# Optimization experiments

Hardware: AMD Instinct MI355X
Metric: run time of the kernel (lower is better)

## Reference

```python
import jax, jax.numpy as jnp
import numpy as np

B, K, D, H = 4, 2048, 768, 12
HD = D // H
NEG = -1e30  # stands in for -inf in the additive mask


def setup_inputs() -> dict:
    key = jax.random.key(0)
    ks = jax.random.split(key, 11)
    s = 1.0 / np.sqrt(D)
    inp = {
        "x": jax.random.normal(ks[0], (B, K, D), jnp.float32),
        "is_context": jax.random.randint(ks[1], (B, K), 0, 2) > 0,
        "Wq": jax.random.normal(ks[2], (D, D), jnp.float32) * s,
        "bq": jax.random.normal(ks[3], (D,), jnp.float32) * 0.01,
        "Wk": jax.random.normal(ks[4], (D, D), jnp.float32) * s,
        "bk": jax.random.normal(ks[5], (D,), jnp.float32) * 0.01,
        "Wv": jax.random.normal(ks[6], (D, D), jnp.float32) * s,
        "bv": jax.random.normal(ks[7], (D,), jnp.float32) * 0.01,
        "Wo": jax.random.normal(ks[8], (D, D), jnp.float32) * s,
        "bo": jax.random.normal(ks[9], (D,), jnp.float32) * 0.01,
    }
    return inp


def reference(x, is_context, Wq, bq, Wk, bk, Wv, bv, Wo, bo):
    b, k_len, d = x.shape
    scale = 1.0 / jnp.sqrt(jnp.asarray(HD, x.dtype))
    # torch nn.Linear: y = x @ W.T + b
    q = (x @ Wq.T + bq).reshape(b, k_len, H, HD).transpose(0, 2, 1, 3)  # [B,H,K,hd]
    kk = (x @ Wk.T + bk).reshape(b, k_len, H, HD).transpose(0, 2, 1, 3)
    v = (x @ Wv.T + bv).reshape(b, k_len, H, HD).transpose(0, 2, 1, 3)

    ctx = is_context  # [B,K] bool
    # allowed[b,i,j]: context rows attend only to context cols; target rows attend to all
    allowed = (ctx[:, :, None] & ctx[:, None, :]) | (~ctx)[:, :, None]  # [B,K,K]

    scores = jnp.einsum("bhqd,bhkd->bhqk", q, kk) * scale  # [B,H,K,K]
    scores = jnp.where(allowed[:, None, :, :], scores, NEG)
    attn = jax.nn.softmax(scores, axis=-1)
    out = jnp.einsum("bhqk,bhkd->bhqd", attn, v)  # [B,H,K,hd]
    out = out.transpose(0, 2, 1, 3).reshape(b, k_len, d)
    return out @ Wo.T + bo
```

## Files before the change

kernel.cpp:

```cpp
#include <hip/hip_runtime.h>
#include <hip/hip_bf16.h>

constexpr int BATCH = 4;
constexpr int SEQ   = 2048;
constexpr int DIM   = 768;
constexpr int NH    = 12;
constexpr int HDIM  = 64;

typedef __attribute__((ext_vector_type(8))) short bf16x8;
typedef __attribute__((ext_vector_type(4))) float f32x4;
typedef __attribute__((ext_vector_type(4))) short s16x4;

__device__ inline short f2bf(float f) {
    union { float f; unsigned u; } v; v.f = f;
    unsigned r = (v.u + 0x7fff + ((v.u >> 16) & 1)) >> 16;
    return (short)r;
}

__device__ inline unsigned pack_bf16x2(float a, float b) {
    union { __hip_bfloat162 h; unsigned u; } c;
    c.h = __float22bfloat162_rn(make_float2(a, b));
    return c.u;
}

__device__ inline float fast_exp2(float x) {
#if __has_builtin(__builtin_amdgcn_exp2f)
    return __builtin_amdgcn_exp2f(x);
#else
    return __expf(x * 0.6931471805599453f);
#endif
}

__device__ inline void gld16(const short* g, short* l) {
    __builtin_amdgcn_global_load_lds(
        (const __attribute__((address_space(1))) void*)g,
        (__attribute__((address_space(3))) void*)l, 16, 0, 0);
}

__device__ inline bool ctx_at(const void* p, bool isU8, int idx) {
    return isU8 ? (((const unsigned char*)p)[idx] != 0)
                : (((const int*)p)[idx] != 0);
}

__global__ __launch_bounds__(256) void prep_kernel(
    const float* __restrict__ x,  const float* __restrict__ Wq,
    const float* __restrict__ Wk, const float* __restrict__ Wv,
    const float* __restrict__ Wo,
    short* __restrict__ xb,  short* __restrict__ Wqb,
    short* __restrict__ Wkb, short* __restrict__ Wvb,
    short* __restrict__ Wob,
    const unsigned char* __restrict__ ctxm, int ctxbytes, int* __restrict__ flag) {
    const int blk = blockIdx.x;
    constexpr int XBLK = (BATCH * SEQ * DIM / 4) / 256;
    constexpr int WBLK = (DIM * DIM / 4) / 256;

    if (blk == XBLK + 4 * WBLK) {
        __shared__ int cnt;
        if (threadIdx.x == 0) cnt = 0;
        __syncthreads();
        int local = 0;
        for (int i = threadIdx.x; i < ctxbytes; i += 256)
            if ((i & 3) != 0 && ctxm[i] != 0) local++;
        atomicAdd(&cnt, local);
        __syncthreads();
        if (threadIdx.x == 0) *flag = (cnt > 0) ? 1 : 0;
        return;
    }

    const float* src; short* dst; int i;
    if (blk < XBLK) {
        src = x; dst = xb;
        i = blk * 256 + threadIdx.x;
    } else {
        const int r = blk - XBLK;
        const int w = r / WBLK;
        src = (w == 0) ? Wq : (w == 1) ? Wk : (w == 2) ? Wv : Wo;
        dst = (w == 0) ? Wqb : (w == 1) ? Wkb : (w == 2) ? Wvb : Wob;
        i = (r - w * WBLK) * 256 + threadIdx.x;
    }
    float4 v = ((const float4*)src)[i];
    s16x4 o;
    o.x = f2bf(v.x); o.y = f2bf(v.y); o.z = f2bf(v.z); o.w = f2bf(v.w);
    ((s16x4*)dst)[i] = o;
}

template <bool BF16OUT>
__global__ __launch_bounds__(256) void gemm_mfma(
    const short* __restrict__ A,
    const short* __restrict__ W0, const float* __restrict__ bias0, void* __restrict__ C0,
    const short* __restrict__ W1, const float* __restrict__ bias1, void* __restrict__ C1,
    const short* __restrict__ W2, const float* __restrict__ bias2, void* __restrict__ C2,
    float scale0) {
    constexpr int N  = DIM;
    constexpr int Kd = DIM;

    const short* W; const float* bias; void* C; float scale;
    if (blockIdx.z == 0)      { W = W0; bias = bias0; C = C0; scale = scale0; }
    else if (blockIdx.z == 1) { W = W1; bias = bias1; C = C1; scale = 1.f; }
    else                      { W = W2; bias = bias2; C = C2; scale = 1.f; }

    const int tid  = threadIdx.x;
    const int wave = tid >> 6;
    const int lane = tid & 63;
    const int quad = lane >> 4;
    const int l16  = lane & 15;
    const int wm   = wave & 1;
    const int wn   = wave >> 1;
    const int m0   = blockIdx.y * 128;
    const int n0   = blockIdx.x * 128;

    __shared__ short As[128 * 32];
    __shared__ short Bs[128 * 32];

    const int srow = tid >> 2;
    const int skq  = tid & 3;
    const short* Ag = A + (size_t)(m0 + srow) * Kd + skq * 8;
    const short* Wg = W + (size_t)(n0 + srow) * Kd + skq * 8;
    short* AsP = As + srow * 32 + skq * 8;
    short* BsP = Bs + srow * 32 + skq * 8;

    f32x4 acc[4][4] = {};

    for (int kt = 0; kt < Kd; kt += 32) {
        __syncthreads();
        gld16(Ag + kt,                AsP);
        gld16(Ag + kt + 64 * Kd,      AsP + 64 * 32);
        gld16(Wg + kt,                BsP);
        gld16(Wg + kt + 64 * Kd,      BsP + 64 * 32);
        __syncthreads();

        bf16x8 af[4], bfr[4];
#pragma unroll
        for (int mt = 0; mt < 4; ++mt)
            af[mt] = *(const bf16x8*)&As[(wm * 64 + mt * 16 + l16) * 32 + quad * 8];
#pragma unroll
        for (int nt = 0; nt < 4; ++nt)
            bfr[nt] = *(const bf16x8*)&Bs[(wn * 64 + nt * 16 + l16) * 32 + quad * 8];
#pragma unroll
        for (int mt = 0; mt < 4; ++mt)
#pragma unroll
            for (int nt = 0; nt < 4; ++nt)
                acc[mt][nt] = __builtin_amdgcn_mfma_f32_16x16x32_bf16(
                    af[mt], bfr[nt], acc[mt][nt], 0, 0, 0);
    }

    float bv[4];
#pragma unroll
    for (int nt = 0; nt < 4; ++nt) bv[nt] = bias[n0 + wn * 64 + nt * 16 + l16];

#pragma unroll
    for (int mt = 0; mt < 4; ++mt)
#pragma unroll
        for (int nt = 0; nt < 4; ++nt)
#pragma unroll
            for (int reg = 0; reg < 4; ++reg) {
                const int m = m0 + wm * 64 + mt * 16 + quad * 4 + reg;
                const int n = n0 + wn * 64 + nt * 16 + l16;
                const float v = (acc[mt][nt][reg] + bv[nt]) * scale;
                if (BF16OUT) ((short*)C)[(size_t)m * N + n] = f2bf(v);
                else         ((float*)C)[(size_t)m * N + n] = v;
            }
}

__global__ __launch_bounds__(256) void vtrans_kernel(
    const short* __restrict__ Vb, short* __restrict__ Vtg) {
    const int b  = blockIdx.z;
    const int h  = blockIdx.y;
    const int k0 = blockIdx.x * 64;
    const int pw = threadIdx.x & 15;
    const int d0 = (threadIdx.x >> 4) * 4;

    const int ks = pw >> 3;
    const int w  = pw & 7;
    const int q  = w >> 1;
    const int kbase = ks * 32 + ((w & 1) ? (16 + (q ^ 2) * 4) : (q * 4));

    s16x4 vr[4];
#pragma unroll
    for (int g = 0; g < 4; ++g)
        vr[g] = *(const s16x4*)(Vb + (size_t)(b * SEQ + k0 + kbase + g) * DIM
                                + h * HDIM + d0);
#pragma unroll
    for (int i = 0; i < 4; ++i) {
        s16x4 o = {vr[0][i], vr[1][i], vr[2][i], vr[3][i]};
        *(s16x4*)(Vtg + (size_t)((b * NH + h) * HDIM + d0 + i) * SEQ + k0 + 4 * pw) = o;
    }
}

__global__ __launch_bounds__(256, 3) void attn_mfma7(
    const short* __restrict__ Qb, const short* __restrict__ Kb,
    const short* __restrict__ Vtg, const void* __restrict__ ctxp,
    const int* __restrict__ flagp, short* __restrict__ Ob) {
    const int b    = blockIdx.z;
    const int h    = blockIdx.y;
    const int q0   = blockIdx.x * 128;
    const int tid  = threadIdx.x;
    const int wave = tid >> 6;
    const int lane = tid & 63;
    const int quad = lane >> 4;
    const int l16  = lane & 15;
    const bool isU8 = (*flagp != 0);

    __shared__ short Ks[2][64 * 64];
    __shared__ short Vs[2][64 * 64];

    const short* Kg = Kb + (size_t)b * SEQ * DIM + h * HDIM;
    const short* Vg = Vtg + (size_t)(b * NH + h) * HDIM * SEQ;

    const int r0 = tid >> 3;
    const int j0 = (tid & 7) ^ (r0 & 7);
    const int sw = l16 & 7;

    bf16x8 qf[2][2];
#pragma unroll
    for (int rg = 0; rg < 2; ++rg) {
        const short* qp = Qb + (size_t)(b * SEQ + q0 + wave * 32 + rg * 16 + l16) * DIM
                        + h * HDIM + quad * 8;
        qf[rg][0] = *(const bf16x8*)qp;
        qf[rg][1] = *(const bf16x8*)(qp + 32);
    }

    unsigned nmb[2];
#pragma unroll
    for (int rg = 0; rg < 2; ++rg)
        nmb[rg] = ctx_at(ctxp, isU8,
            b * SEQ + q0 + wave * 32 + rg * 16 + l16) ? 0u : 0xFFFFFFFFu;

    bf16x8 ones;
#pragma unroll
    for (int i = 0; i < 8; ++i) ones[i] = (short)0x3F80;

    f32x4 accl[2] = {};
    f32x4 acc[2][4] = {};

    {
        gld16(Kg + (size_t)r0 * DIM + j0 * 8,        &Ks[0][tid * 8]);
        gld16(Kg + (size_t)(r0 + 32) * DIM + j0 * 8, &Ks[0][(tid + 256) * 8]);
        gld16(Vg + (size_t)r0 * SEQ + j0 * 8,        &Vs[0][tid * 8]);
        gld16(Vg + (size_t)(r0 + 32) * SEQ + j0 * 8, &Vs[0][(tid + 256) * 8]);
    }

    constexpr int NT = SEQ / 64;
    for (int t = 0; t < NT; ++t) {
        const int k0  = t * 64;
        const int cur = t & 1;

        __syncthreads();

        if (t + 1 < NT) {
            const int kn  = k0 + 64;
            const int nxt = cur ^ 1;
            gld16(Kg + (size_t)(kn + r0) * DIM + j0 * 8,        &Ks[nxt][tid * 8]);
            gld16(Kg + (size_t)(kn + r0 + 32) * DIM + j0 * 8,   &Ks[nxt][(tid + 256) * 8]);
            gld16(Vg + (size_t)r0 * SEQ + kn + j0 * 8,          &Vs[nxt][tid * 8]);
            gld16(Vg + (size_t)(r0 + 32) * SEQ + kn + j0 * 8,   &Vs[nxt][(tid + 256) * 8]);
        }

        const short* BK = Ks[cur];
        const short* BV = Vs[cur];

        const unsigned long long kmask =
            __ballot(ctx_at(ctxp, isU8, b * SEQ + k0 + lane));

        f32x4 s4[4][2] = {};
        __builtin_amdgcn_s_setprio(1);
#pragma unroll
        for (int ks = 0; ks < 2; ++ks) {
            bf16x8 kf[4];
#pragma unroll
            for (int g = 0; g < 4; ++g)
                kf[g] = *(const bf16x8*)
                    &BK[(g * 16 + l16) * 64 + (((ks * 4 + quad) ^ sw)) * 8];
#pragma unroll
            for (int g = 0; g < 4; ++g) {
                s4[g][0] = __builtin_amdgcn_mfma_f32_16x16x32_bf16(kf[g], qf[0][ks], s4[g][0], 0, 0, 0);
                s4[g][1] = __builtin_amdgcn_mfma_f32_16x16x32_bf16(kf[g], qf[1][ks], s4[g][1], 0, 0, 0);
            }
        }
        __builtin_amdgcn_s_setprio(0);

        unsigned mw[2][4];
#pragma unroll
        for (int ks = 0; ks < 2; ++ks)
#pragma unroll
            for (int w = 0; w < 4; ++w) {
                const int base = 32 * ks + ((w >> 1) & 1) * 16 + quad * 4 + (w & 1) * 2;
                const unsigned two = (unsigned)(kmask >> base) & 3u;
                mw[ks][w] = ((two & 1u) ? 0x0000FFFFu : 0u) |
                            ((two & 2u) ? 0xFFFF0000u : 0u);
            }

        bf16x8 pa[2][2];
#pragma unroll
        for (int rg = 0; rg < 2; ++rg) {
            const unsigned nm = nmb[rg];
#pragma unroll
            for (int ks = 0; ks < 2; ++ks) {
                const int g0 = 2 * ks, g1 = 2 * ks + 1;
                const float e0 = fast_exp2(s4[g0][rg][0]);
                const float e1 = fast_exp2(s4[g0][rg][1]);
                const float e2 = fast_exp2(s4[g0][rg][2]);
                const float e3 = fast_exp2(s4[g0][rg][3]);
                const float e4 = fast_exp2(s4[g1][rg][0]);
                const float e5 = fast_exp2(s4[g1][rg][1]);
                const float e6 = fast_exp2(s4[g1][rg][2]);
                const float e7 = fast_exp2(s4[g1][rg][3]);
                const unsigned wA0 = pack_bf16x2(e0, e1) & (nm | mw[ks][0]);
                const unsigned wA1 = pack_bf16x2(e2, e3) & (nm | mw[ks][1]);
                const unsigned wB0 = pack_bf16x2(e4, e5) & (nm | mw[ks][2]);
                const unsigned wB1 = pack_bf16x2(e6, e7) & (nm | mw[ks][3]);
                const unsigned pB0 = (unsigned)__shfl((int)wB0, lane ^ 32);
                const unsigned pB1 = (unsigned)__shfl((int)wB1, lane ^ 32);
                union { bf16x8 v; unsigned u[4]; } tb;
                tb.u[0] = wA0; tb.u[1] = wA1; tb.u[2] = pB0; tb.u[3] = pB1;
                pa[rg][ks] = tb.v;
            }
        }

        __builtin_amdgcn_s_setprio(1);
#pragma unroll
        for (int ks = 0; ks < 2; ++ks) {
            accl[0] = __builtin_amdgcn_mfma_f32_16x16x32_bf16(pa[0][ks], ones, accl[0], 0, 0, 0);
            accl[1] = __builtin_amdgcn_mfma_f32_16x16x32_bf16(pa[1][ks], ones, accl[1], 0, 0, 0);
#pragma unroll
            for (int dt = 0; dt < 4; ++dt) {
                bf16x8 vf = *(const bf16x8*)
                    &BV[(dt * 16 + l16) * 64 + (((ks * 4 + quad) ^ sw)) * 8];
                acc[0][dt] = __builtin_amdgcn_mfma_f32_16x16x32_bf16(pa[0][ks], vf, acc[0][dt], 0, 0, 0);
                acc[1][dt] = __builtin_amdgcn_mfma_f32_16x16x32_bf16(pa[1][ks], vf, acc[1][dt], 0, 0, 0);
            }
        }
        __builtin_amdgcn_s_setprio(0);
    }

    float inv[2][4];
#pragma unroll
    for (int rg = 0; rg < 2; ++rg)
#pragma unroll
        for (int reg = 0; reg < 4; ++reg)
            inv[rg][reg] = 1.f / accl[rg][reg];

#pragma unroll
    for (int rg = 0; rg < 2; ++rg)
#pragma unroll
        for (int dt = 0; dt < 4; ++dt)
#pragma unroll
            for (int reg = 0; reg < 4; ++reg) {
                const int q = q0 + wave * 32 + rg * 16 + quad * 4 + reg;
                Ob[(size_t)(b * SEQ + q) * DIM + h * HDIM + dt * 16 + l16] =
                    f2bf(acc[rg][dt][reg] * inv[rg][reg]);
            }
}

extern "C" void kernel_launch(void* const* d_in, const int* in_sizes, int n_in,
                              void* d_out, int out_size, void* d_ws, size_t ws_size,
                              hipStream_t stream) {
    const float* x   = (const float*)d_in[0];
    const void*  ctx = d_in[1];
    const float* Wq  = (const float*)d_in[2];
    const float* bq  = (const float*)d_in[3];
    const float* Wk  = (const float*)d_in[4];
    const float* bk  = (const float*)d_in[5];
    const float* Wv  = (const float*)d_in[6];
    const float* bv  = (const float*)d_in[7];
    const float* Wo  = (const float*)d_in[8];
    const float* bo  = (const float*)d_in[9];
    float* out = (float*)d_out;

    char* ws = (char*)d_ws;
    int* flag = (int*)ws;
    const size_t bufbf = (size_t)BATCH * SEQ * DIM * sizeof(short);
    const size_t wbuf  = (size_t)DIM * DIM * sizeof(short);
    short* xb  = (short*)(ws + 256);
    short* Qb  = (short*)(ws + 256 + bufbf);
    short* Kb  = (short*)(ws + 256 + 2 * bufbf);
    short* Vb  = (short*)(ws + 256 + 3 * bufbf);
    short* Ab  = (short*)(ws + 256 + 4 * bufbf);
    short* Vtg = (short*)(ws + 256 + 5 * bufbf);
    short* Wqb = (short*)(ws + 256 + 6 * bufbf);
    short* Wkb = (short*)(ws + 256 + 6 * bufbf + wbuf);
    short* Wvb = (short*)(ws + 256 + 6 * bufbf + 2 * wbuf);
    short* Wob = (short*)(ws + 256 + 6 * bufbf + 3 * wbuf);

    constexpr int XBLK = (BATCH * SEQ * DIM / 4) / 256;
    constexpr int WBLK = (DIM * DIM / 4) / 256;
    prep_kernel<<<XBLK + 4 * WBLK + 1, 256, 0, stream>>>(
        x, Wq, Wk, Wv, Wo, xb, Wqb, Wkb, Wvb, Wob,
        (const unsigned char*)ctx, BATCH * SEQ, flag);

    dim3 gQKV(DIM / 128, (BATCH * SEQ) / 128, 3);
    gemm_mfma<true><<<gQKV, 256, 0, stream>>>(
        xb, Wqb, bq, Qb, Wkb, bk, Kb, Wvb, bv, Vb, 0.125f * 1.4426950408889634f);

    dim3 gVt(SEQ / 64, NH, BATCH);
    vtrans_kernel<<<gVt, 256, 0, stream>>>(Vb, Vtg);

    dim3 gAttn(SEQ / 128, NH, BATCH);
    attn_mfma7<<<gAttn, 256, 0, stream>>>(Qb, Kb, Vtg, ctx, flag, Ab);

    dim3 gOut(DIM / 128, (BATCH * SEQ) / 128, 1);
    gemm_mfma<false><<<gOut, 256, 0, stream>>>(
        Ab, Wob, bo, out, Wob, bo, out, Wob, bo, out, 1.f);
}
```

Measured before the change: 259.8 us.

## Triple-buffer K/V tiles with explicit vmcnt waits and swizzle attention grid

```diff
diff --git a/kernel.cpp b/kernel.cpp
--- a/kernel.cpp
+++ b/kernel.cpp
@@ -187,13 +187,15 @@
     }
 }
 
-__global__ __launch_bounds__(256, 3) void attn_mfma7(
+__global__ __launch_bounds__(256, 3) void attn_mfma8(
     const short* __restrict__ Qb, const short* __restrict__ Kb,
     const short* __restrict__ Vtg, const void* __restrict__ ctxp,
     const int* __restrict__ flagp, short* __restrict__ Ob) {
-    const int b    = blockIdx.z;
-    const int h    = blockIdx.y;
-    const int q0   = blockIdx.x * 128;
+    const int swz  = (blockIdx.x & 7) * 96 + (blockIdx.x >> 3);
+    const int qc   = swz & 15;
+    const int h    = (swz >> 4) % NH;
+    const int b    = swz / (16 * NH);
+    const int q0   = qc * 128;
     const int tid  = threadIdx.x;
     const int wave = tid >> 6;
     const int lane = tid & 63;
@@ -201,8 +203,8 @@
     const int l16  = lane & 15;
     const bool isU8 = (*flagp != 0);
 
-    __shared__ short Ks[2][64 * 64];
-    __shared__ short Vs[2][64 * 64];
+    __shared__ short Ks[3][64 * 64];
+    __shared__ short Vs[3][64 * 64];
 
     const short* Kg = Kb + (size_t)b * SEQ * DIM + h * HDIM;
     const short* Vg = Vtg + (size_t)(b * NH + h) * HDIM * SEQ;
@@ -226,6 +228,11 @@
         nmb[rg] = ctx_at(ctxp, isU8,
             b * SEQ + q0 + wave * 32 + rg * 16 + l16) ? 0u : 0xFFFFFFFFu;
 
+    constexpr int NT = SEQ / 64;
+    unsigned kbits = 0;
+    for (int t = 0; t < NT; ++t)
+        kbits |= (ctx_at(ctxp, isU8, b * SEQ + t * 64 + lane) ? 1u : 0u) << t;
+
     bf16x8 ones;
 #pragma unroll
     for (int i = 0; i < 8; ++i) ones[i] = (short)0x3F80;
@@ -233,34 +240,35 @@
     f32x4 accl[2] = {};
     f32x4 acc[2][4] = {};
 
-    {
-        gld16(Kg + (size_t)r0 * DIM + j0 * 8,        &Ks[0][tid * 8]);
-        gld16(Kg + (size_t)(r0 + 32) * DIM + j0 * 8, &Ks[0][(tid + 256) * 8]);
-        gld16(Vg + (size_t)r0 * SEQ + j0 * 8,        &Vs[0][tid * 8]);
-        gld16(Vg + (size_t)(r0 + 32) * SEQ + j0 * 8, &Vs[0][(tid + 256) * 8]);
-    }
-
-    constexpr int NT = SEQ / 64;
+    auto stage = [&](int t) {
+        short* KD = Ks[t % 3];
+        short* VD = Vs[t % 3];
+        const int kn = t * 64;
+        gld16(Kg + (size_t)(kn + r0) * DIM + j0 * 8,      KD + tid * 8);
+        gld16(Kg + (size_t)(kn + r0 + 32) * DIM + j0 * 8, KD + (tid + 256) * 8);
+        gld16(Vg + (size_t)r0 * SEQ + kn + j0 * 8,        VD + tid * 8);
+        gld16(Vg + (size_t)(r0 + 32) * SEQ + kn + j0 * 8, VD + (tid + 256) * 8);
+    };
+
+    stage(0);
+    stage(1);
+
     for (int t = 0; t < NT; ++t) {
-        const int k0  = t * 64;
-        const int cur = t & 1;
-
-        __syncthreads();
-
-        if (t + 1 < NT) {
-            const int kn  = k0 + 64;
-            const int nxt = cur ^ 1;
-            gld16(Kg + (size_t)(kn + r0) * DIM + j0 * 8,        &Ks[nxt][tid * 8]);
-            gld16(Kg + (size_t)(kn + r0 + 32) * DIM + j0 * 8,   &Ks[nxt][(tid + 256) * 8]);
-            gld16(Vg + (size_t)r0 * SEQ + kn + j0 * 8,          &Vs[nxt][tid * 8]);
-            gld16(Vg + (size_t)(r0 + 32) * SEQ + kn + j0 * 8,   &Vs[nxt][(tid + 256) * 8]);
-        }
-
-        const short* BK = Ks[cur];
-        const short* BV = Vs[cur];
-
-        const unsigned long long kmask =
-            __ballot(ctx_at(ctxp, isU8, b * SEQ + k0 + lane));
+        const short* BK = Ks[t % 3];
+        const short* BV = Vs[t % 3];
+
+        __builtin_amdgcn_s_barrier();
+        __builtin_amdgcn_sched_barrier(0);
+        if (t + 2 < NT) stage(t + 2);
+
+        if (t < NT - 2)       asm volatile("s_waitcnt vmcnt(8)" ::: "memory");
+        else if (t == NT - 2) asm volatile("s_waitcnt vmcnt(4)" ::: "memory");
+        else                  asm volatile("s_waitcnt vmcnt(0)" ::: "memory");
+        __builtin_amdgcn_sched_barrier(0);
+        __builtin_amdgcn_s_barrier();
+        __builtin_amdgcn_sched_barrier(0);
+
+        const unsigned long long kmask = __ballot((kbits >> t) & 1u);
 
         f32x4 s4[4][2] = {};
         __builtin_amdgcn_s_setprio(1);
@@ -395,8 +403,8 @@
     dim3 gVt(SEQ / 64, NH, BATCH);
     vtrans_kernel<<<gVt, 256, 0, stream>>>(Vb, Vtg);
 
-    dim3 gAttn(SEQ / 128, NH, BATCH);
-    attn_mfma7<<<gAttn, 256, 0, stream>>>(Qb, Kb, Vtg, ctx, flag, Ab);
+    attn_mfma8<<<dim3(SEQ / 128 * NH * BATCH, 1, 1), 256, 0, stream>>>(
+        Qb, Kb, Vtg, ctx, flag, Ab);
 
     dim3 gOut(DIM / 128, (BATCH * SEQ) / 128, 1);
     gemm_mfma<false><<<gOut, 256, 0, stream>>>(
```

Result: no change. 258.7 us (-0.4%).

## Widen GEMM K-tile with swizzled LDS, remap blocks for XCD locality, raise attention occupancy

Applied to the files above, without the earlier changes.

```diff
diff --git a/kernel.cpp b/kernel.cpp
--- a/kernel.cpp
+++ b/kernel.cpp
@@ -84,7 +84,7 @@
     ((s16x4*)dst)[i] = o;
 }
 
-template <bool BF16OUT>
+template <bool BF16OUT, int NSPLIT>
 __global__ __launch_bounds__(256) void gemm_mfma(
     const short* __restrict__ A,
     const short* __restrict__ W0, const float* __restrict__ bias0, void* __restrict__ C0,
@@ -93,11 +93,22 @@
     float scale0) {
     constexpr int N  = DIM;
     constexpr int Kd = DIM;
+    constexpr int MT = (BATCH * SEQ) / 128;
+    constexpr int NTL = DIM / 128;
+    constexpr int TOT = MT * NTL * NSPLIT;
+    constexpr int CHUNK = TOT / 8;
+
+    const int bid = blockIdx.x;
+    const int L = (bid & 7) * CHUNK + (bid >> 3);
+    const int m_idx = L / (NTL * NSPLIT);
+    const int rr    = L % (NTL * NSPLIT);
+    const int n_idx = rr % NTL;
+    const int z     = rr / NTL;
 
     const short* W; const float* bias; void* C; float scale;
-    if (blockIdx.z == 0)      { W = W0; bias = bias0; C = C0; scale = scale0; }
-    else if (blockIdx.z == 1) { W = W1; bias = bias1; C = C1; scale = 1.f; }
-    else                      { W = W2; bias = bias2; C = C2; scale = 1.f; }
+    if (z == 0)      { W = W0; bias = bias0; C = C0; scale = scale0; }
+    else if (z == 1) { W = W1; bias = bias1; C = C1; scale = 1.f; }
+    else             { W = W2; bias = bias2; C = C2; scale = 1.f; }
 
     const int tid  = threadIdx.x;
     const int wave = tid >> 6;
@@ -106,42 +117,49 @@
     const int l16  = lane & 15;
     const int wm   = wave & 1;
     const int wn   = wave >> 1;
-    const int m0   = blockIdx.y * 128;
-    const int n0   = blockIdx.x * 128;
-
-    __shared__ short As[128 * 32];
-    __shared__ short Bs[128 * 32];
-
-    const int srow = tid >> 2;
-    const int skq  = tid & 3;
-    const short* Ag = A + (size_t)(m0 + srow) * Kd + skq * 8;
-    const short* Wg = W + (size_t)(n0 + srow) * Kd + skq * 8;
-    short* AsP = As + srow * 32 + skq * 8;
-    short* BsP = Bs + srow * 32 + skq * 8;
+    const int m0   = m_idx * 128;
+    const int n0   = n_idx * 128;
+
+    __shared__ short As[128 * 64];
+    __shared__ short Bs[128 * 64];
+
+    const int srow = tid >> 3;
+    const int j    = tid & 7;
+    const int j0   = j ^ (srow & 7);
+    const int sw   = l16 & 7;
+
+    const short* Ag = A + (size_t)(m0 + srow) * Kd + j0 * 8;
+    const short* Wg = W + (size_t)(n0 + srow) * Kd + j0 * 8;
 
     f32x4 acc[4][4] = {};
 
-    for (int kt = 0; kt < Kd; kt += 32) {
+    for (int kt = 0; kt < Kd; kt += 64) {
         __syncthreads();
-        gld16(Ag + kt,                AsP);
-        gld16(Ag + kt + 64 * Kd,      AsP + 64 * 32);
-        gld16(Wg + kt,                BsP);
-        gld16(Wg + kt + 64 * Kd,      BsP + 64 * 32);
+#pragma unroll
+        for (int p = 0; p < 4; ++p) {
+            gld16(Ag + (size_t)(p * 32) * Kd + kt, As + p * 2048 + tid * 8);
+            gld16(Wg + (size_t)(p * 32) * Kd + kt, Bs + p * 2048 + tid * 8);
+        }
         __syncthreads();
 
-        bf16x8 af[4], bfr[4];
-#pragma unroll
-        for (int mt = 0; mt < 4; ++mt)
-            af[mt] = *(const bf16x8*)&As[(wm * 64 + mt * 16 + l16) * 32 + quad * 8];
-#pragma unroll
-        for (int nt = 0; nt < 4; ++nt)
-            bfr[nt] = *(const bf16x8*)&Bs[(wn * 64 + nt * 16 + l16) * 32 + quad * 8];
-#pragma unroll
-        for (int mt = 0; mt < 4; ++mt)
+#pragma unroll
+        for (int ks2 = 0; ks2 < 2; ++ks2) {
+            bf16x8 af[4], bfr[4];
+#pragma unroll
+            for (int mt = 0; mt < 4; ++mt)
+                af[mt] = *(const bf16x8*)
+                    &As[(wm * 64 + mt * 16 + l16) * 64 + ((ks2 * 4 + quad) ^ sw) * 8];
 #pragma unroll
             for (int nt = 0; nt < 4; ++nt)
-                acc[mt][nt] = __builtin_amdgcn_mfma_f32_16x16x32_bf16(
-                    af[mt], bfr[nt], acc[mt][nt], 0, 0, 0);
+                bfr[nt] = *(const bf16x8*)
+                    &Bs[(wn * 64 + nt * 16 + l16) * 64 + ((ks2 * 4 + quad) ^ sw) * 8];
+#pragma unroll
+            for (int mt = 0; mt < 4; ++mt)
+#pragma unroll
+                for (int nt = 0; nt < 4; ++nt)
+                    acc[mt][nt] = __builtin_amdgcn_mfma_f32_16x16x32_bf16(
+                        af[mt], bfr[nt], acc[mt][nt], 0, 0, 0);
+        }
     }
 
     float bv[4];
@@ -187,13 +205,15 @@
     }
 }
 
-__global__ __launch_bounds__(256, 3) void attn_mfma7(
+__global__ __launch_bounds__(256, 5) void attn_mfma11(
     const short* __restrict__ Qb, const short* __restrict__ Kb,
     const short* __restrict__ Vtg, const void* __restrict__ ctxp,
     const int* __restrict__ flagp, short* __restrict__ Ob) {
-    const int b    = blockIdx.z;
-    const int h    = blockIdx.y;
-    const int q0   = blockIdx.x * 128;
+    const int swz  = (blockIdx.x & 7) * 96 + (blockIdx.x >> 3);
+    const int qc   = swz & 15;
+    const int h    = (swz >> 4) % NH;
+    const int b    = swz / (16 * NH);
+    const int q0   = qc * 128;
     const int tid  = threadIdx.x;
     const int wave = tid >> 6;
     const int lane = tid & 63;
@@ -388,17 +408,17 @@
         x, Wq, Wk, Wv, Wo, xb, Wqb, Wkb, Wvb, Wob,
         (const unsigned char*)ctx, BATCH * SEQ, flag);
 
-    dim3 gQKV(DIM / 128, (BATCH * SEQ) / 128, 3);
-    gemm_mfma<true><<<gQKV, 256, 0, stream>>>(
+    gemm_mfma<true, 3><<<dim3((DIM / 128) * ((BATCH * SEQ) / 128) * 3, 1, 1),
+                          256, 0, stream>>>(
         xb, Wqb, bq, Qb, Wkb, bk, Kb, Wvb, bv, Vb, 0.125f * 1.4426950408889634f);
 
     dim3 gVt(SEQ / 64, NH, BATCH);
     vtrans_kernel<<<gVt, 256, 0, stream>>>(Vb, Vtg);
 
-    dim3 gAttn(SEQ / 128, NH, BATCH);
-    attn_mfma7<<<gAttn, 256, 0, stream>>>(Qb, Kb, Vtg, ctx, flag, Ab);
-
-    dim3 gOut(DIM / 128, (BATCH * SEQ) / 128, 1);
-    gemm_mfma<false><<<gOut, 256, 0, stream>>>(
+    attn_mfma11<<<dim3(SEQ / 128 * NH * BATCH, 1, 1), 256, 0, stream>>>(
+        Qb, Kb, Vtg, ctx, flag, Ab);
+
+    gemm_mfma<false, 1><<<dim3((DIM / 128) * ((BATCH * SEQ) / 128), 1, 1),
+                           256, 0, stream>>>(
         Ab, Wob, bo, out, Wob, bo, out, Wob, bo, out, 1.f);
 }
```

Measured after the change: 432.2 us. 66.4% more time.
